# Optimization experiments

Measured on AMD Instinct MI355X. Metric: run time of the kernel, lower is better.

Reference implementation:

```python
import jax, jax.numpy as jnp
import numpy as np

INPUT_SIZE = 512
HIDDEN_SIZE = 1024


def _xavier(key, shape):
    fan_in, fan_out = shape
    limit = np.sqrt(6.0 / (fan_in + fan_out))
    return jax.random.uniform(key, shape, jnp.float32, -limit, limit)


def setup_inputs() -> dict:
    key = jax.random.key(0)
    ks = jax.random.split(key, 9)
    N, S, F, H = 256, 512, INPUT_SIZE, HIDDEN_SIZE
    return {
        "x": jax.random.normal(ks[0], (N, S, F), jnp.float32),
        "Wii": _xavier(ks[1], (F, H)), "Whi": _xavier(ks[2], (H, H)), "bi": jnp.zeros((H,), jnp.float32),
        "Wif": _xavier(ks[3], (F, H)), "Whf": _xavier(ks[4], (H, H)), "bf": jnp.zeros((H,), jnp.float32),
        "Wig": _xavier(ks[5], (F, H)), "Whg": _xavier(ks[6], (H, H)), "bg": jnp.zeros((H,), jnp.float32),
        "Wio": _xavier(ks[7], (F, H)), "Who": _xavier(ks[8], (H, H)), "bo": jnp.zeros((H,), jnp.float32),
    }


def reference(x, Wii, Whi, bi, Wif, Whf, bf, Wig, Whg, bg, Wio, Who, bo):
    N, S, F = x.shape
    H = Whi.shape[0]
    # Fuse the 4 input-to-hidden GEMMs into one big batched GEMM over all timesteps.
    Wi = jnp.concatenate([Wii, Wif, Wig, Wio], axis=1)            # [F, 4H]
    Wh = jnp.concatenate([Whi, Whf, Whg, Who], axis=1)            # [H, 4H]
    b = jnp.concatenate([bi, bf, bg, bo], axis=0)                 # [4H]
    x_proj = jnp.einsum('nsf,fg->sng', x, Wi) + b                 # [S, N, 4H]

    def step(carry, xp_t):
        h, c = carry
        gates = xp_t + h @ Wh                                     # [N, 4H]
        i_t = jax.nn.sigmoid(gates[:, 0 * H:1 * H])
        f_t = jax.nn.sigmoid(gates[:, 1 * H:2 * H])
        g_t = jnp.tanh(gates[:, 2 * H:3 * H])
        o_t = jax.nn.sigmoid(gates[:, 3 * H:4 * H])
        c = i_t * g_t + f_t * c
        h = o_t * jnp.tanh(c)
        return (h, c), None

    h0 = jnp.zeros((N, H), x.dtype)
    c0 = jnp.zeros((N, H), x.dtype)
    (h_t, c_t), _ = jax.lax.scan(step, (h0, c0), x_proj)
    return (h_t, c_t)
```

## Files before the change

kernel.cpp:

```cpp
#include <hip/hip_runtime.h>
#include <hip/hip_bf16.h>
#include <stdint.h>


typedef __bf16 bf16x8 __attribute__((ext_vector_type(8)));
typedef float  f32x4  __attribute__((ext_vector_type(4)));
typedef float  f32x2  __attribute__((ext_vector_type(2)));
typedef uint32_t u32x4 __attribute__((ext_vector_type(4)));

union U8 { bf16x8 v; __bf16 e[8]; };
union PK { uint32_t u; __bf16 e[2]; };

#define MFMA16(a,b,c) __builtin_amdgcn_mfma_f32_16x16x32_bf16((a),(b),(c),0,0,0)

#define GLOADX4(dst, base, OFF)                                              \
  asm volatile("global_load_dwordx4 %0, %1, off offset:" #OFF " sc0 sc1"     \
               : "=v"(dst) : "v"(base))
#define GSTORE1(base, val)                                                   \
  asm volatile("global_store_dword %0, %1, off sc0 sc1"                      \
               :: "v"(base), "v"(val) : "memory")
#define WAIT_VM0() asm volatile("s_waitcnt vmcnt(0)" ::: "memory")

__global__ __launch_bounds__(512, 2) void lstm_persist(
    const float* __restrict__ x,
    const float* __restrict__ Wii, const float* __restrict__ Whi, const float* __restrict__ bi,
    const float* __restrict__ Wif, const float* __restrict__ Whf, const float* __restrict__ bfv,
    const float* __restrict__ Wig, const float* __restrict__ Whg, const float* __restrict__ bgv,
    const float* __restrict__ Wio, const float* __restrict__ Who, const float* __restrict__ bov,
    float* __restrict__ out,
    uint32_t* __restrict__ hbuf,
    uint32_t* cnts)
{
  constexpr int S = 512;
  __shared__ uint32_t hsu[32 * 516];
  __shared__ float    Pbuf[8192];
  __shared__ __bf16   transb[32 * 33];

  const int wg   = blockIdx.x;
  const int rb   = wg >> 5;
  const int cb   = wg & 31;
  const int tid  = threadIdx.x;
  const int wv   = tid >> 6;
  const int g    = wv & 3;
  const int hf   = wv >> 2;
  const int lane = tid & 63;
  const int l15  = lane & 15;
  const int quad = lane >> 4;

  uint32_t* const mycnt = cnts + rb * 256;

  const float* Wi_g = (g == 0) ? Wii : (g == 1) ? Wif : (g == 2) ? Wig : Wio;
  const float* Wh_g = (g == 0) ? Whi : (g == 1) ? Whf : (g == 2) ? Whg : Who;

  bf16x8 hB[16][2];
  bf16x8 xB[8][2];
  #pragma unroll
  for (int nt = 0; nt < 2; ++nt) {
    const int col = cb * 32 + nt * 16 + l15;
    #pragma unroll
    for (int kt = 0; kt < 16; ++kt) {
      U8 u;
      #pragma unroll
      for (int j = 0; j < 8; ++j)
        u.e[j] = (__bf16)Wh_g[(size_t)(hf * 512 + kt * 32 + quad * 8 + j) * 1024 + col];
      hB[kt][nt] = u.v;
    }
    #pragma unroll
    for (int kt = 0; kt < 8; ++kt) {
      U8 u;
      #pragma unroll
      for (int j = 0; j < 8; ++j)
        u.e[j] = (__bf16)Wi_g[(size_t)(hf * 256 + kt * 32 + quad * 8 + j) * 1024 + col];
      xB[kt][nt] = u.v;
    }
  }

  const int acc_r  = (tid >> 7) & 3;
  const int rp_r   = (tid >> 6) & 1;
  const int mt_r   = acc_r >> 1, nt_r = acc_r & 1;
  const int col_l  = nt_r * 16 + l15;
  const int row0_l = mt_r * 16 + quad * 4 + rp_r * 2;
  const int gcol   = cb * 32 + col_l;
  const int grow0  = rb * 32 + row0_l;
  const float bias_i = bi[gcol], bias_f = bfv[gcol];
  const float bias_g = bgv[gcol], bias_o = bov[gcol];
  float cc0 = 0.f, cc1 = 0.f;

  uint32_t* const hb0 = hbuf;
  uint32_t* const hb1 = hbuf + 131072;

  const float* xr0 = x + (size_t)(rb * 32 + l15) * (512 * 512) + hf * 256 + quad * 8;
  const float* xr1 = xr0 + (size_t)16 * (512 * 512);

  const int crow = tid >> 4, cseg = tid & 15;
  uint32_t* const ldst = hsu + crow * 516 + cseg * 4;
  const size_t gofs = (size_t)(rb * 32 + crow) * 512 + cseg * 4;

  const uint32_t* hA0 = hsu + l15 * 516 + hf * 256 + quad * 4;
  const uint32_t* hA1 = hsu + (l15 + 16) * 516 + hf * 256 + quad * 4;

  const int srow = tid >> 4, scol = (tid & 15) * 2;
  const size_t sdst = (size_t)(rb * 32 + srow) * 512 + cb * 16 + (tid & 15);

  for (int t = 0; t < S; ++t) {
    f32x4 a00 = {0,0,0,0}, a01 = {0,0,0,0}, a10 = {0,0,0,0}, a11 = {0,0,0,0};

    const float* p0 = xr0 + (size_t)t * 512;
    const float* p1 = xr1 + (size_t)t * 512;
    #pragma unroll
    for (int kt = 0; kt < 8; ++kt) {
      const float4 u0 = *(const float4*)(p0 + kt * 32);
      const float4 u1 = *(const float4*)(p0 + kt * 32 + 4);
      const float4 v0 = *(const float4*)(p1 + kt * 32);
      const float4 v1 = *(const float4*)(p1 + kt * 32 + 4);
      U8 A0, A1;
      A0.e[0]=(__bf16)u0.x; A0.e[1]=(__bf16)u0.y; A0.e[2]=(__bf16)u0.z; A0.e[3]=(__bf16)u0.w;
      A0.e[4]=(__bf16)u1.x; A0.e[5]=(__bf16)u1.y; A0.e[6]=(__bf16)u1.z; A0.e[7]=(__bf16)u1.w;
      A1.e[0]=(__bf16)v0.x; A1.e[1]=(__bf16)v0.y; A1.e[2]=(__bf16)v0.z; A1.e[3]=(__bf16)v0.w;
      A1.e[4]=(__bf16)v1.x; A1.e[5]=(__bf16)v1.y; A1.e[6]=(__bf16)v1.z; A1.e[7]=(__bf16)v1.w;
      a00 = MFMA16(A0.v, xB[kt][0], a00);  a01 = MFMA16(A0.v, xB[kt][1], a01);
      a10 = MFMA16(A1.v, xB[kt][0], a10);  a11 = MFMA16(A1.v, xB[kt][1], a11);
    }

    if (tid == 0) {
      const uint32_t target = (uint32_t)t * 32u;
      while (__hip_atomic_load(mycnt, __ATOMIC_RELAXED, __HIP_MEMORY_SCOPE_AGENT) < target)
        __builtin_amdgcn_s_sleep(1);
    }
    __syncthreads();

    {
      const uint32_t* hcur = ((t & 1) ? hb1 : hb0) + gofs;
      u32x4 tv0, tv1, tv2, tv3, tv4, tv5, tv6, tv7;
      GLOADX4(tv0, hcur, 0);    GLOADX4(tv1, hcur, 256);
      GLOADX4(tv2, hcur, 512);  GLOADX4(tv3, hcur, 768);
      GLOADX4(tv4, hcur, 1024); GLOADX4(tv5, hcur, 1280);
      GLOADX4(tv6, hcur, 1536); GLOADX4(tv7, hcur, 1792);
      WAIT_VM0();
      *(u32x4*)(ldst +   0) = tv0;  *(u32x4*)(ldst +  64) = tv1;
      *(u32x4*)(ldst + 128) = tv2;  *(u32x4*)(ldst + 192) = tv3;
      *(u32x4*)(ldst + 256) = tv4;  *(u32x4*)(ldst + 320) = tv5;
      *(u32x4*)(ldst + 384) = tv6;  *(u32x4*)(ldst + 448) = tv7;
    }
    __syncthreads();

    #pragma unroll
    for (int kt = 0; kt < 16; ++kt) {
      const bf16x8 A0 = *(const bf16x8*)(hA0 + kt * 16);
      const bf16x8 A1 = *(const bf16x8*)(hA1 + kt * 16);
      a00 = MFMA16(A0, hB[kt][0], a00);  a01 = MFMA16(A0, hB[kt][1], a01);
      a10 = MFMA16(A1, hB[kt][0], a10);  a11 = MFMA16(A1, hB[kt][1], a11);
    }

    *(f32x4*)&Pbuf[(wv * 4 + 0) * 256 + lane * 4] = a00;
    *(f32x4*)&Pbuf[(wv * 4 + 1) * 256 + lane * 4] = a01;
    *(f32x4*)&Pbuf[(wv * 4 + 2) * 256 + lane * 4] = a10;
    *(f32x4*)&Pbuf[(wv * 4 + 3) * 256 + lane * 4] = a11;
    __syncthreads();

    const int off = acc_r * 256 + lane * 4 + rp_r * 2;
    const f32x2 qi = *(const f32x2*)&Pbuf[0 * 1024 + off];
    const f32x2 ri = *(const f32x2*)&Pbuf[4 * 1024 + off];
    const f32x2 qf = *(const f32x2*)&Pbuf[1 * 1024 + off];
    const f32x2 rf = *(const f32x2*)&Pbuf[5 * 1024 + off];
    const f32x2 qg = *(const f32x2*)&Pbuf[2 * 1024 + off];
    const f32x2 rg = *(const f32x2*)&Pbuf[6 * 1024 + off];
    const f32x2 qo = *(const f32x2*)&Pbuf[3 * 1024 + off];
    const f32x2 ro = *(const f32x2*)&Pbuf[7 * 1024 + off];

    float hn0, hn1;
    {
      const float pi0 = qi[0] + ri[0] + bias_i, pi1 = qi[1] + ri[1] + bias_i;
      const float pf0 = qf[0] + rf[0] + bias_f, pf1 = qf[1] + rf[1] + bias_f;
      const float pg0 = qg[0] + rg[0] + bias_g, pg1 = qg[1] + rg[1] + bias_g;
      const float po0 = qo[0] + ro[0] + bias_o, po1 = qo[1] + ro[1] + bias_o;
      const float gi0 = __builtin_amdgcn_rcpf(1.f + __expf(-pi0));
      const float gi1 = __builtin_amdgcn_rcpf(1.f + __expf(-pi1));
      const float gf0 = __builtin_amdgcn_rcpf(1.f + __expf(-pf0));
      const float gf1 = __builtin_amdgcn_rcpf(1.f + __expf(-pf1));
      const float gg0 = 2.f * __builtin_amdgcn_rcpf(1.f + __expf(-2.f * pg0)) - 1.f;
      const float gg1 = 2.f * __builtin_amdgcn_rcpf(1.f + __expf(-2.f * pg1)) - 1.f;
      const float go0 = __builtin_amdgcn_rcpf(1.f + __expf(-po0));
      const float go1 = __builtin_amdgcn_rcpf(1.f + __expf(-po1));
      cc0 = gi0 * gg0 + gf0 * cc0;
      cc1 = gi1 * gg1 + gf1 * cc1;
      const float tc0 = 2.f * __builtin_amdgcn_rcpf(1.f + __expf(-2.f * cc0)) - 1.f;
      const float tc1 = 2.f * __builtin_amdgcn_rcpf(1.f + __expf(-2.f * cc1)) - 1.f;
      hn0 = go0 * tc0;
      hn1 = go1 * tc1;
      transb[(row0_l + 0) * 33 + col_l] = (__bf16)hn0;
      transb[(row0_l + 1) * 33 + col_l] = (__bf16)hn1;
    }
    __syncthreads();

    {
      PK pk;
      pk.e[0] = transb[srow * 33 + scol];
      pk.e[1] = transb[srow * 33 + scol + 1];
      uint32_t* dst = ((t & 1) ? hb0 : hb1) + sdst;
      GSTORE1(dst, pk.u);
    }
    if (t == S - 1) {
      out[(size_t)(grow0 + 0) * 1024 + gcol] = hn0;
      out[(size_t)(grow0 + 1) * 1024 + gcol] = hn1;
      out[262144 + (size_t)(grow0 + 0) * 1024 + gcol] = cc0;
      out[262144 + (size_t)(grow0 + 1) * 1024 + gcol] = cc1;
    }
    WAIT_VM0();
    __syncthreads();
    if (tid == 0)
      __hip_atomic_fetch_add(mycnt, 1u, __ATOMIC_RELAXED, __HIP_MEMORY_SCOPE_AGENT);
  }
}

extern "C" void kernel_launch(void* const* d_in, const int* in_sizes, int n_in,
                              void* d_out, int out_size, void* d_ws, size_t ws_size,
                              hipStream_t stream) {
  const float* xp  = (const float*)d_in[0];
  const float* Wii = (const float*)d_in[1];
  const float* Whi = (const float*)d_in[2];
  const float* bi  = (const float*)d_in[3];
  const float* Wif = (const float*)d_in[4];
  const float* Whf = (const float*)d_in[5];
  const float* bf_ = (const float*)d_in[6];
  const float* Wig = (const float*)d_in[7];
  const float* Whg = (const float*)d_in[8];
  const float* bg  = (const float*)d_in[9];
  const float* Wio = (const float*)d_in[10];
  const float* Who = (const float*)d_in[11];
  const float* bo  = (const float*)d_in[12];
  float* out = (float*)d_out;

  uint32_t* hbuf = (uint32_t*)d_ws;
  uint32_t* cnts = (uint32_t*)((char*)d_ws + 2u * 262144u * sizeof(__bf16));

  hipMemsetAsync(d_ws, 0, 2u * 262144u * sizeof(__bf16) + 8u * 1024u, stream);

  lstm_persist<<<dim3(256), dim3(512), 0, stream>>>(
      xp, Wii, Whi, bi, Wif, Whf, bf_, Wig, Whg, bg, Wio, Who, bo,
      out, hbuf, cnts);
}
```

Baseline: 6.031 ms.

## Split each row block into two independent 16-row streams with separate counters

Each workgroup now processes its 32 batch rows as two 16-row sub-blocks, each with its own cross-workgroup counter, so waiting on one half's hidden state can overlap with work on the other. The hidden-state staging is laid out in shared memory directly in MFMA fragment order to avoid the padded row layout, and the global h loads are issued before the input-projection MFMAs to hide latency. The trade-off is twice as many barriers and atomic handshakes per timestep, and half the threads sit idle during the store phase.

```diff
diff --git a/kernel.cpp b/kernel.cpp
--- a/kernel.cpp
+++ b/kernel.cpp
@@ -5,7 +5,6 @@
 
 typedef __bf16 bf16x8 __attribute__((ext_vector_type(8)));
 typedef float  f32x4  __attribute__((ext_vector_type(4)));
-typedef float  f32x2  __attribute__((ext_vector_type(2)));
 typedef uint32_t u32x4 __attribute__((ext_vector_type(4)));
 
 union U8 { bf16x8 v; __bf16 e[8]; };
@@ -32,9 +31,9 @@
     uint32_t* cnts)
 {
   constexpr int S = 512;
-  __shared__ uint32_t hsu[32 * 516];
-  __shared__ float    Pbuf[8192];
-  __shared__ __bf16   transb[32 * 33];
+  __shared__ uint32_t hfrag[2][8192];
+  __shared__ float    Pbuf[4096];
+  __shared__ __bf16   transb[16 * 34];
 
   const int wg   = blockIdx.x;
   const int rb   = wg >> 5;
@@ -47,8 +46,6 @@
   const int l15  = lane & 15;
   const int quad = lane >> 4;
 
-  uint32_t* const mycnt = cnts + rb * 256;
-
   const float* Wi_g = (g == 0) ? Wii : (g == 1) ? Wif : (g == 2) ? Wig : Wio;
   const float* Wh_g = (g == 0) ? Whi : (g == 1) ? Whf : (g == 2) ? Whg : Who;
 
@@ -75,141 +72,126 @@
     }
   }
 
-  const int acc_r  = (tid >> 7) & 3;
-  const int rp_r   = (tid >> 6) & 1;
-  const int mt_r   = acc_r >> 1, nt_r = acc_r & 1;
-  const int col_l  = nt_r * 16 + l15;
-  const int row0_l = mt_r * 16 + quad * 4 + rp_r * 2;
-  const int gcol   = cb * 32 + col_l;
-  const int grow0  = rb * 32 + row0_l;
+  const int nt_r  = (tid >> 4) & 1;
+  const int reg_r = (tid >> 5) & 3;
+  const int q_r   = (tid >> 7) & 3;
+  const int rcol  = nt_r * 16 + l15 - (quad >> 2) * 0 + 0;
+  const int col_l = nt_r * 16 + (tid & 15);
+  const int row_l = q_r * 4 + reg_r;
+  const int gcol  = cb * 32 + col_l;
   const float bias_i = bi[gcol], bias_f = bfv[gcol];
   const float bias_g = bgv[gcol], bias_o = bov[gcol];
-  float cc0 = 0.f, cc1 = 0.f;
+  float cc[2] = {0.f, 0.f};
+  (void)rcol;
+
+  const int wr_r = tid & 15;
+  const int wr_j = tid >> 4;
+  const int wbase = ((wr_j & 3) * 16 + wr_r) * 4 + (wr_j >> 2) * 256;
+
+  const int srow = (tid >> 4) & 15, scd = tid & 15;
 
   uint32_t* const hb0 = hbuf;
   uint32_t* const hb1 = hbuf + 131072;
 
-  const float* xr0 = x + (size_t)(rb * 32 + l15) * (512 * 512) + hf * 256 + quad * 8;
-  const float* xr1 = xr0 + (size_t)16 * (512 * 512);
-
-  const int crow = tid >> 4, cseg = tid & 15;
-  uint32_t* const ldst = hsu + crow * 516 + cseg * 4;
-  const size_t gofs = (size_t)(rb * 32 + crow) * 512 + cseg * 4;
-
-  const uint32_t* hA0 = hsu + l15 * 516 + hf * 256 + quad * 4;
-  const uint32_t* hA1 = hsu + (l15 + 16) * 516 + hf * 256 + quad * 4;
-
-  const int srow = tid >> 4, scol = (tid & 15) * 2;
-  const size_t sdst = (size_t)(rb * 32 + srow) * 512 + cb * 16 + (tid & 15);
+  __syncthreads();
 
   for (int t = 0; t < S; ++t) {
-    f32x4 a00 = {0,0,0,0}, a01 = {0,0,0,0}, a10 = {0,0,0,0}, a11 = {0,0,0,0};
-
-    const float* p0 = xr0 + (size_t)t * 512;
-    const float* p1 = xr1 + (size_t)t * 512;
     #pragma unroll
-    for (int kt = 0; kt < 8; ++kt) {
-      const float4 u0 = *(const float4*)(p0 + kt * 32);
-      const float4 u1 = *(const float4*)(p0 + kt * 32 + 4);
-      const float4 v0 = *(const float4*)(p1 + kt * 32);
-      const float4 v1 = *(const float4*)(p1 + kt * 32 + 4);
-      U8 A0, A1;
-      A0.e[0]=(__bf16)u0.x; A0.e[1]=(__bf16)u0.y; A0.e[2]=(__bf16)u0.z; A0.e[3]=(__bf16)u0.w;
-      A0.e[4]=(__bf16)u1.x; A0.e[5]=(__bf16)u1.y; A0.e[6]=(__bf16)u1.z; A0.e[7]=(__bf16)u1.w;
-      A1.e[0]=(__bf16)v0.x; A1.e[1]=(__bf16)v0.y; A1.e[2]=(__bf16)v0.z; A1.e[3]=(__bf16)v0.w;
-      A1.e[4]=(__bf16)v1.x; A1.e[5]=(__bf16)v1.y; A1.e[6]=(__bf16)v1.z; A1.e[7]=(__bf16)v1.w;
-      a00 = MFMA16(A0.v, xB[kt][0], a00);  a01 = MFMA16(A0.v, xB[kt][1], a01);
-      a10 = MFMA16(A1.v, xB[kt][0], a10);  a11 = MFMA16(A1.v, xB[kt][1], a11);
+    for (int s = 0; s < 2; ++s) {
+      const int rbase = rb * 32 + s * 16;
+      uint32_t* const mycnt = cnts + (rb * 2 + s) * 256;
+
+      const float* px = x + (size_t)(rbase + l15) * (512 * 512)
+                          + (size_t)t * 512 + hf * 256 + quad * 8;
+      U8 xA[8];
+      #pragma unroll
+      for (int kt = 0; kt < 8; ++kt) {
+        const float4 u0 = *(const float4*)(px + kt * 32);
+        const float4 u1 = *(const float4*)(px + kt * 32 + 4);
+        xA[kt].e[0]=(__bf16)u0.x; xA[kt].e[1]=(__bf16)u0.y;
+        xA[kt].e[2]=(__bf16)u0.z; xA[kt].e[3]=(__bf16)u0.w;
+        xA[kt].e[4]=(__bf16)u1.x; xA[kt].e[5]=(__bf16)u1.y;
+        xA[kt].e[6]=(__bf16)u1.z; xA[kt].e[7]=(__bf16)u1.w;
+      }
+
+      if (tid == 0) {
+        const uint32_t target = (uint32_t)t * 32u;
+        while (__hip_atomic_load(mycnt, __ATOMIC_RELAXED, __HIP_MEMORY_SCOPE_AGENT) < target)
+          __builtin_amdgcn_s_sleep(1);
+      }
+      __syncthreads();
+
+      const uint32_t* hsrc = ((t & 1) ? hb1 : hb0)
+                             + (size_t)(rbase + wr_r) * 512 + wr_j * 4;
+      u32x4 h0, h1, h2, h3;
+      GLOADX4(h0, hsrc, 0);
+      GLOADX4(h1, hsrc, 512);
+      GLOADX4(h2, hsrc, 1024);
+      GLOADX4(h3, hsrc, 1536);
+
+      f32x4 a0 = {0,0,0,0}, a1 = {0,0,0,0};
+      #pragma unroll
+      for (int kt = 0; kt < 8; ++kt) {
+        a0 = MFMA16(xA[kt].v, xB[kt][0], a0);
+        a1 = MFMA16(xA[kt].v, xB[kt][1], a1);
+      }
+
+      WAIT_VM0();
+      {
+        uint32_t* hw = &hfrag[s][0] + wbase;
+        *(u32x4*)(hw +    0) = h0;
+        *(u32x4*)(hw + 2048) = h1;
+        *(u32x4*)(hw + 4096) = h2;
+        *(u32x4*)(hw + 6144) = h3;
+      }
+      __syncthreads();
+
+      const uint32_t* hr = &hfrag[s][0] + hf * 16 * 256 + lane * 4;
+      #pragma unroll
+      for (int kt = 0; kt < 16; ++kt) {
+        const bf16x8 A = *(const bf16x8*)(hr + kt * 256);
+        a0 = MFMA16(A, hB[kt][0], a0);
+        a1 = MFMA16(A, hB[kt][1], a1);
+      }
+
+      *(f32x4*)&Pbuf[(wv * 2 + 0) * 256 + lane * 4] = a0;
+      *(f32x4*)&Pbuf[(wv * 2 + 1) * 256 + lane * 4] = a1;
+      __syncthreads();
+
+      const int po = (q_r * 16 + (tid & 15)) * 4 + reg_r;
+      const float pi = Pbuf[(0 + nt_r) * 256 + po] + Pbuf[( 8 + nt_r) * 256 + po] + bias_i;
+      const float pf = Pbuf[(2 + nt_r) * 256 + po] + Pbuf[(10 + nt_r) * 256 + po] + bias_f;
+      const float pg = Pbuf[(4 + nt_r) * 256 + po] + Pbuf[(12 + nt_r) * 256 + po] + bias_g;
+      const float pob= Pbuf[(6 + nt_r) * 256 + po] + Pbuf[(14 + nt_r) * 256 + po] + bias_o;
+
+      const float gi = __builtin_amdgcn_rcpf(1.f + __expf(-pi));
+      const float gf = __builtin_amdgcn_rcpf(1.f + __expf(-pf));
+      const float gg = 2.f * __builtin_amdgcn_rcpf(1.f + __expf(-2.f * pg)) - 1.f;
+      const float go = __builtin_amdgcn_rcpf(1.f + __expf(-pob));
+      const float cn = gi * gg + gf * cc[s];
+      cc[s] = cn;
+      const float tc = 2.f * __builtin_amdgcn_rcpf(1.f + __expf(-2.f * cn)) - 1.f;
+      const float hn = go * tc;
+      transb[row_l * 34 + col_l] = (__bf16)hn;
+      if (t == S - 1) {
+        out[(size_t)(rbase + row_l) * 1024 + gcol] = hn;
+        out[262144 + (size_t)(rbase + row_l) * 1024 + gcol] = cn;
+      }
+      __syncthreads();
+
+      if (tid < 256) {
+        PK pk;
+        pk.e[0] = transb[srow * 34 + scd * 2];
+        pk.e[1] = transb[srow * 34 + scd * 2 + 1];
+        uint32_t* dst = ((t & 1) ? hb0 : hb1)
+                        + (size_t)(rbase + srow) * 512 + cb * 16 + scd;
+        GSTORE1(dst, pk.u);
+      }
+      WAIT_VM0();
+      __syncthreads();
+      if (tid == 0)
+        __hip_atomic_fetch_add(mycnt, 1u, __ATOMIC_RELAXED, __HIP_MEMORY_SCOPE_AGENT);
     }
-
-    if (tid == 0) {
-      const uint32_t target = (uint32_t)t * 32u;
-      while (__hip_atomic_load(mycnt, __ATOMIC_RELAXED, __HIP_MEMORY_SCOPE_AGENT) < target)
-        __builtin_amdgcn_s_sleep(1);
-    }
-    __syncthreads();
-
-    {
-      const uint32_t* hcur = ((t & 1) ? hb1 : hb0) + gofs;
-      u32x4 tv0, tv1, tv2, tv3, tv4, tv5, tv6, tv7;
-      GLOADX4(tv0, hcur, 0);    GLOADX4(tv1, hcur, 256);
-      GLOADX4(tv2, hcur, 512);  GLOADX4(tv3, hcur, 768);
-      GLOADX4(tv4, hcur, 1024); GLOADX4(tv5, hcur, 1280);
-      GLOADX4(tv6, hcur, 1536); GLOADX4(tv7, hcur, 1792);
-      WAIT_VM0();
-      *(u32x4*)(ldst +   0) = tv0;  *(u32x4*)(ldst +  64) = tv1;
-      *(u32x4*)(ldst + 128) = tv2;  *(u32x4*)(ldst + 192) = tv3;
-      *(u32x4*)(ldst + 256) = tv4;  *(u32x4*)(ldst + 320) = tv5;
-      *(u32x4*)(ldst + 384) = tv6;  *(u32x4*)(ldst + 448) = tv7;
-    }
-    __syncthreads();
-
-    #pragma unroll
-    for (int kt = 0; kt < 16; ++kt) {
-      const bf16x8 A0 = *(const bf16x8*)(hA0 + kt * 16);
-      const bf16x8 A1 = *(const bf16x8*)(hA1 + kt * 16);
-      a00 = MFMA16(A0, hB[kt][0], a00);  a01 = MFMA16(A0, hB[kt][1], a01);
-      a10 = MFMA16(A1, hB[kt][0], a10);  a11 = MFMA16(A1, hB[kt][1], a11);
-    }
-
-    *(f32x4*)&Pbuf[(wv * 4 + 0) * 256 + lane * 4] = a00;
-    *(f32x4*)&Pbuf[(wv * 4 + 1) * 256 + lane * 4] = a01;
-    *(f32x4*)&Pbuf[(wv * 4 + 2) * 256 + lane * 4] = a10;
-    *(f32x4*)&Pbuf[(wv * 4 + 3) * 256 + lane * 4] = a11;
-    __syncthreads();
-
-    const int off = acc_r * 256 + lane * 4 + rp_r * 2;
-    const f32x2 qi = *(const f32x2*)&Pbuf[0 * 1024 + off];
-    const f32x2 ri = *(const f32x2*)&Pbuf[4 * 1024 + off];
-    const f32x2 qf = *(const f32x2*)&Pbuf[1 * 1024 + off];
-    const f32x2 rf = *(const f32x2*)&Pbuf[5 * 1024 + off];
-    const f32x2 qg = *(const f32x2*)&Pbuf[2 * 1024 + off];
-    const f32x2 rg = *(const f32x2*)&Pbuf[6 * 1024 + off];
-    const f32x2 qo = *(const f32x2*)&Pbuf[3 * 1024 + off];
-    const f32x2 ro = *(const f32x2*)&Pbuf[7 * 1024 + off];
-
-    float hn0, hn1;
-    {
-      const float pi0 = qi[0] + ri[0] + bias_i, pi1 = qi[1] + ri[1] + bias_i;
-      const float pf0 = qf[0] + rf[0] + bias_f, pf1 = qf[1] + rf[1] + bias_f;
-      const float pg0 = qg[0] + rg[0] + bias_g, pg1 = qg[1] + rg[1] + bias_g;
-      const float po0 = qo[0] + ro[0] + bias_o, po1 = qo[1] + ro[1] + bias_o;
-      const float gi0 = __builtin_amdgcn_rcpf(1.f + __expf(-pi0));
-      const float gi1 = __builtin_amdgcn_rcpf(1.f + __expf(-pi1));
-      const float gf0 = __builtin_amdgcn_rcpf(1.f + __expf(-pf0));
-      const float gf1 = __builtin_amdgcn_rcpf(1.f + __expf(-pf1));
-      const float gg0 = 2.f * __builtin_amdgcn_rcpf(1.f + __expf(-2.f * pg0)) - 1.f;
-      const float gg1 = 2.f * __builtin_amdgcn_rcpf(1.f + __expf(-2.f * pg1)) - 1.f;
-      const float go0 = __builtin_amdgcn_rcpf(1.f + __expf(-po0));
-      const float go1 = __builtin_amdgcn_rcpf(1.f + __expf(-po1));
-      cc0 = gi0 * gg0 + gf0 * cc0;
-      cc1 = gi1 * gg1 + gf1 * cc1;
-      const float tc0 = 2.f * __builtin_amdgcn_rcpf(1.f + __expf(-2.f * cc0)) - 1.f;
-      const float tc1 = 2.f * __builtin_amdgcn_rcpf(1.f + __expf(-2.f * cc1)) - 1.f;
-      hn0 = go0 * tc0;
-      hn1 = go1 * tc1;
-      transb[(row0_l + 0) * 33 + col_l] = (__bf16)hn0;
-      transb[(row0_l + 1) * 33 + col_l] = (__bf16)hn1;
-    }
-    __syncthreads();
-
-    {
-      PK pk;
-      pk.e[0] = transb[srow * 33 + scol];
-      pk.e[1] = transb[srow * 33 + scol + 1];
-      uint32_t* dst = ((t & 1) ? hb0 : hb1) + sdst;
-      GSTORE1(dst, pk.u);
-    }
-    if (t == S - 1) {
-      out[(size_t)(grow0 + 0) * 1024 + gcol] = hn0;
-      out[(size_t)(grow0 + 1) * 1024 + gcol] = hn1;
-      out[262144 + (size_t)(grow0 + 0) * 1024 + gcol] = cc0;
-      out[262144 + (size_t)(grow0 + 1) * 1024 + gcol] = cc1;
-    }
-    WAIT_VM0();
-    __syncthreads();
-    if (tid == 0)
-      __hip_atomic_fetch_add(mycnt, 1u, __ATOMIC_RELAXED, __HIP_MEMORY_SCOPE_AGENT);
   }
 }
 
@@ -234,7 +216,7 @@
   uint32_t* hbuf = (uint32_t*)d_ws;
   uint32_t* cnts = (uint32_t*)((char*)d_ws + 2u * 262144u * sizeof(__bf16));
 
-  hipMemsetAsync(d_ws, 0, 2u * 262144u * sizeof(__bf16) + 8u * 1024u, stream);
+  hipMemsetAsync(d_ws, 0, 2u * 262144u * sizeof(__bf16) + 16u * 1024u, stream);
 
   lstm_persist<<<dim3(256), dim3(512), 0, stream>>>(
       xp, Wii, Whi, bi, Wif, Whf, bf_, Wig, Whg, bg, Wio, Who, bo,
```

Result: slower. 10.08 ms (+67.2%).
